# Performance work log

Hardware: AMD Instinct MI355X
Metric: run time of the kernel (lower is better)

## Reference

```python
import jax, jax.numpy as jnp
import numpy as np
from jax import lax

B, D, H, STEPS = 16384, 256, 256, 25


def setup_inputs() -> dict:
    key = jax.random.key(0)
    k1, k2, k3, k4 = jax.random.split(key, 4)
    s1 = 1.0 / np.sqrt(D)
    s2 = 1.0 / np.sqrt(H)
    return {
        "z0": jax.random.normal(k1, (B, D), dtype=jnp.float32),
        "t_range": jnp.linspace(0.0, 1.0, STEPS, dtype=jnp.float32),
        "W1": jax.random.normal(k2, (D, H), dtype=jnp.float32) * s1,
        "b1": jnp.zeros((H,), dtype=jnp.float32),
        "wt": jax.random.normal(k3, (H,), dtype=jnp.float32) * 0.1,
        "W2": jax.random.normal(k4, (H, D), dtype=jnp.float32) * s2,
        "b2": jnp.zeros((D,), dtype=jnp.float32),
    }


def reference(z0, t_range, W1, b1, wt, W2, b2):
    # Euler solver: zt <- zt + dt * f(zt, t) for every t in t_range
    # (matches euler_solver: note it steps at ALL 25 grid points, incl. t_end)
    dt = t_range[1] - t_range[0]

    def dynamics(z, t):
        h = jnp.tanh(z @ W1 + b1 + t * wt)  # [B, H]
        return h @ W2 + b2                   # [B, D]

    def step(z, t):
        return z + dt * dynamics(z, t), None

    zT, _ = lax.scan(step, z0, t_range)
    return zT
```

## Files before the change

### kernel.cpp

```cpp
#include <hip/hip_runtime.h>

typedef short bf16x8 __attribute__((ext_vector_type(8)));
typedef float f32x4  __attribute__((ext_vector_type(4)));

#define NSTEP 25
#define SROW  264
#define LDSB  (32 * SROW)

__device__ __forceinline__ unsigned short f2bf(float x) {
    union { float f; unsigned int u; } v; v.f = x;
    unsigned int r = v.u + 0x7FFFu + ((v.u >> 16) & 1u);
    return (unsigned short)(r >> 16);
}

#if __has_builtin(__builtin_amdgcn_cvt_pk_bf16_f32)
typedef __bf16 bfv2 __attribute__((ext_vector_type(2)));
__device__ __forceinline__ unsigned int pk2bf(float a, float b) {
    union { bfv2 v; unsigned int u; } c;
    c.v = __builtin_amdgcn_cvt_pk_bf16_f32(a, b);
    return c.u;
}
#else
__device__ __forceinline__ unsigned int pk2bf(float a, float b) {
    return (unsigned int)f2bf(a) | ((unsigned int)f2bf(b) << 16);
}
#endif

__device__ __forceinline__ float tanh_fast(float x) {
    float e = __expf(2.0f * x);
    return 1.0f - 2.0f * __builtin_amdgcn_rcpf(e + 1.0f);
}

__global__ void prep_all(const float* __restrict__ W1,
                         const float* __restrict__ W2,
                         const float* __restrict__ b2,
                         const float* __restrict__ t_range,
                         unsigned short* __restrict__ Wr,
                         unsigned short* __restrict__ W21r,
                         float* __restrict__ c1)
{
    __shared__ float row[256];
    int b = blockIdx.x;
    if (b < 512) {
        const float* src = (b < 256) ? W1 : W2;
        unsigned short* dst = Wr + ((b < 256) ? 0 : 65536);
        int k = b & 255;
        int n = threadIdx.x;
        int p  = (k & ~31) | ((k & 15) << 1) | ((k >> 4) & 1);
        int kc = p >> 5, q = (p >> 3) & 3, j = p & 7;
        dst[kc * 8192 + n * 32 + q * 8 + j] = f2bf(src[k * 256 + n]);
    } else {
        int i = b - 512, j = threadIdx.x;
        row[j] = (i < 256) ? W2[i * 256 + j] : b2[j];
        __syncthreads();
        float acc = 0.f;
        for (int d = 0; d < 256; ++d)
            acc = fmaf(row[d], W1[d * 256 + j], acc);
        if (i < 256) {
            float dt = t_range[1] - t_range[0];
            int p  = (i & ~31) | ((i & 15) << 1) | ((i >> 4) & 1);
            int kc = p >> 5, q = (p >> 3) & 3, jj = p & 7;
            W21r[kc * 8192 + j * 32 + q * 8 + jj] = f2bf(dt * acc);
        } else {
            c1[j] = acc;
        }
    }
}

__global__ __launch_bounds__(512, 4) void ode_main(
    const float* __restrict__ z0,
    const float* __restrict__ t_range,
    const float* __restrict__ b1,
    const float* __restrict__ wt,
    const float* __restrict__ b2,
    const unsigned short* __restrict__ W1r,
    const unsigned short* __restrict__ W2r,
    const unsigned short* __restrict__ W21r,
    const float* __restrict__ c1,
    float* __restrict__ out)
{
    __shared__ __align__(16) unsigned short As[2 * LDSB];

    const int tid  = threadIdx.x;
    const int wave = tid >> 6;
    const int lane = tid & 63;
    const int q    = lane >> 4;
    const int l15  = lane & 15;
    const int row0 = blockIdx.x * 32;
    const int n0   = wave * 32;

    const float dt = t_range[1] - t_range[0];

    float bt[2], dbt[2];
#pragma unroll
    for (int tt = 0; tt < 2; ++tt) {
        int n = n0 + tt * 16 + l15;
        bt[tt]  = b1[n];
        dbt[tt] = dt * (wt[n] + c1[n]);
    }

#pragma unroll
    for (int band = 0; band < 2; ++band)
#pragma unroll
        for (int r = 0; r < 4; ++r) {
            int m = band * 16 + q * 4 + r;
            const float* zr = &z0[(row0 + m) * 256 + n0];
            *(unsigned int*)&As[m * SROW + n0 + l15 * 2] =
                pk2bf(zr[l15], zr[16 + l15]);
        }
    __syncthreads();

    f32x4 y[2][2];
#pragma unroll
    for (int band = 0; band < 2; ++band)
#pragma unroll
        for (int tt = 0; tt < 2; ++tt) y[band][tt] = f32x4{0.f, 0.f, 0.f, 0.f};
#pragma unroll
    for (int kc = 0; kc < 8; ++kc) {
        bf16x8 a[2];
#pragma unroll
        for (int band = 0; band < 2; ++band)
            a[band] = *(const bf16x8*)&As[(band * 16 + l15) * SROW + kc * 32 + q * 8];
#pragma unroll
        for (int tt = 0; tt < 2; ++tt) {
            bf16x8 bb = *(const bf16x8*)&W1r[kc * 8192 + (n0 + tt * 16 + l15) * 32 + q * 8];
#pragma unroll
            for (int band = 0; band < 2; ++band)
                y[band][tt] = __builtin_amdgcn_mfma_f32_16x16x32_bf16(
                    a[band], bb, y[band][tt], 0, 0, 0);
        }
    }

    bf16x8 w21f[8][2];
#pragma unroll
    for (int kc = 0; kc < 8; ++kc)
#pragma unroll
        for (int tt = 0; tt < 2; ++tt)
            w21f[kc][tt] = *(const bf16x8*)&W21r[kc * 8192 + (n0 + tt * 16 + l15) * 32 + q * 8];

    f32x4 S[2][2];
#pragma unroll
    for (int band = 0; band < 2; ++band)
#pragma unroll
        for (int tt = 0; tt < 2; ++tt) S[band][tt] = f32x4{0.f, 0.f, 0.f, 0.f};

    for (int s = 0; s < NSTEP - 1; ++s) {
        const int buf = ((s + 1) & 1) * LDSB;
#pragma unroll
        for (int band = 0; band < 2; ++band)
#pragma unroll
            for (int r = 0; r < 4; ++r) {
                int m = band * 16 + q * 4 + r;
                float h0 = tanh_fast(y[band][0][r] + bt[0]);
                float h1 = tanh_fast(y[band][1][r] + bt[1]);
                S[band][0][r] += h0; S[band][1][r] += h1;
                *(unsigned int*)&As[buf + m * SROW + n0 + l15 * 2] = pk2bf(h0, h1);
            }
        __syncthreads();

#pragma unroll
        for (int kc = 0; kc < 8; ++kc) {
            bf16x8 a[2];
#pragma unroll
            for (int band = 0; band < 2; ++band)
                a[band] = *(const bf16x8*)&As[buf + (band * 16 + l15) * SROW + kc * 32 + q * 8];
#pragma unroll
            for (int band = 0; band < 2; ++band)
#pragma unroll
                for (int tt = 0; tt < 2; ++tt)
                    y[band][tt] = __builtin_amdgcn_mfma_f32_16x16x32_bf16(
                        a[band], w21f[kc][tt], y[band][tt], 0, 0, 0);
        }

#pragma unroll
        for (int tt = 0; tt < 2; ++tt) bt[tt] += dbt[tt];
    }

#pragma unroll
    for (int band = 0; band < 2; ++band)
#pragma unroll
        for (int r = 0; r < 4; ++r)
#pragma unroll
            for (int tt = 0; tt < 2; ++tt)
                S[band][tt][r] += tanh_fast(y[band][tt][r] + bt[tt]);

    {
        const int buf = LDSB;
#pragma unroll
        for (int band = 0; band < 2; ++band)
#pragma unroll
            for (int r = 0; r < 4; ++r) {
                int m = band * 16 + q * 4 + r;
                *(unsigned int*)&As[buf + m * SROW + n0 + l15 * 2] =
                    pk2bf(S[band][0][r], S[band][1][r]);
            }
        __syncthreads();

        f32x4 acc[2][2];
#pragma unroll
        for (int band = 0; band < 2; ++band)
#pragma unroll
            for (int tt = 0; tt < 2; ++tt) acc[band][tt] = f32x4{0.f, 0.f, 0.f, 0.f};
#pragma unroll
        for (int kc = 0; kc < 8; ++kc) {
            bf16x8 a[2];
#pragma unroll
            for (int band = 0; band < 2; ++band)
                a[band] = *(const bf16x8*)&As[buf + (band * 16 + l15) * SROW + kc * 32 + q * 8];
#pragma unroll
            for (int tt = 0; tt < 2; ++tt) {
                bf16x8 bb = *(const bf16x8*)&W2r[kc * 8192 + (n0 + tt * 16 + l15) * 32 + q * 8];
#pragma unroll
                for (int band = 0; band < 2; ++band)
                    acc[band][tt] = __builtin_amdgcn_mfma_f32_16x16x32_bf16(
                        a[band], bb, acc[band][tt], 0, 0, 0);
            }
        }

        const float cb2 = (float)NSTEP * dt;
#pragma unroll
        for (int band = 0; band < 2; ++band)
#pragma unroll
            for (int tt = 0; tt < 2; ++tt) {
                float b2v = b2[n0 + tt * 16 + l15];
#pragma unroll
                for (int r = 0; r < 4; ++r) {
                    int idx = (row0 + band * 16 + q * 4 + r) * 256 + n0 + tt * 16 + l15;
                    out[idx] = z0[idx] + dt * acc[band][tt][r] + cb2 * b2v;
                }
            }
    }
}

extern "C" void kernel_launch(void* const* d_in, const int* in_sizes, int n_in,
                              void* d_out, int out_size, void* d_ws, size_t ws_size,
                              hipStream_t stream) {
    const float* z0      = (const float*)d_in[0];
    const float* t_range = (const float*)d_in[1];
    const float* W1      = (const float*)d_in[2];
    const float* b1      = (const float*)d_in[3];
    const float* wt      = (const float*)d_in[4];
    const float* W2      = (const float*)d_in[5];
    const float* b2      = (const float*)d_in[6];

    unsigned short* Wr = (unsigned short*)d_ws;
    unsigned short* W1r  = Wr;
    unsigned short* W2r  = Wr + 65536;
    unsigned short* W21r = Wr + 131072;
    float*          c1   = (float*)(Wr + 196608);

    prep_all<<<769, 256, 0, stream>>>(W1, W2, b2, t_range, Wr, W21r, c1);
    ode_main<<<512, 512, 0, stream>>>(z0, t_range, b1, wt, b2,
                                      W1r, W2r, W21r, c1, (float*)d_out);
}
```

Measured before the change: 152.9 us.

## Replace block barriers with per-wave LDS flags and rotated k-chunk order

Each __syncthreads in the ODE loop is replaced by per-wave monotonic flags in LDS. Each wave publishes its slice of the tanh activations and starts the MFMA reduction on its own k-chunk first, then spin-waits with s_sleep only for the other chunks it needs. The goal is to cut the full-block barrier stall each Euler step, so fast waves can overlap with slow ones. The W21 fragment loads move before the first GEMM, and the prep reduction gets four independent accumulators to shorten its dependency chain. The spin-wait polling and fences may cost more than the barriers they replace.

```diff
diff --git a/kernel.cpp b/kernel.cpp
--- a/kernel.cpp
+++ b/kernel.cpp
@@ -29,6 +29,12 @@
 __device__ __forceinline__ float tanh_fast(float x) {
     float e = __expf(2.0f * x);
     return 1.0f - 2.0f * __builtin_amdgcn_rcpf(e + 1.0f);
+}
+
+__device__ __forceinline__ void wait_flag(const unsigned int* f, unsigned int v) {
+    while (__hip_atomic_load(f, __ATOMIC_RELAXED, __HIP_MEMORY_SCOPE_WORKGROUP) < v)
+        __builtin_amdgcn_s_sleep(1);
+    __threadfence_block();
 }
 
 __global__ void prep_all(const float* __restrict__ W1,
@@ -53,9 +59,14 @@
         int i = b - 512, j = threadIdx.x;
         row[j] = (i < 256) ? W2[i * 256 + j] : b2[j];
         __syncthreads();
-        float acc = 0.f;
-        for (int d = 0; d < 256; ++d)
-            acc = fmaf(row[d], W1[d * 256 + j], acc);
+        float a0 = 0.f, a1 = 0.f, a2 = 0.f, a3 = 0.f;
+        for (int d = 0; d < 256; d += 4) {
+            a0 = fmaf(row[d    ], W1[(d    ) * 256 + j], a0);
+            a1 = fmaf(row[d + 1], W1[(d + 1) * 256 + j], a1);
+            a2 = fmaf(row[d + 2], W1[(d + 2) * 256 + j], a2);
+            a3 = fmaf(row[d + 3], W1[(d + 3) * 256 + j], a3);
+        }
+        float acc = (a0 + a1) + (a2 + a3);
         if (i < 256) {
             float dt = t_range[1] - t_range[0];
             int p  = (i & ~31) | ((i & 15) << 1) | ((i >> 4) & 1);
@@ -80,6 +91,7 @@
     float* __restrict__ out)
 {
     __shared__ __align__(16) unsigned short As[2 * LDSB];
+    __shared__ unsigned int flags[8];
 
     const int tid  = threadIdx.x;
     const int wave = tid >> 6;
@@ -89,8 +101,9 @@
     const int row0 = blockIdx.x * 32;
     const int n0   = wave * 32;
 
+    if (tid < 8) flags[tid] = 0;
+
     const float dt = t_range[1] - t_range[0];
-
     float bt[2], dbt[2];
 #pragma unroll
     for (int tt = 0; tt < 2; ++tt) {
@@ -98,6 +111,8 @@
         bt[tt]  = b1[n];
         dbt[tt] = dt * (wt[n] + c1[n]);
     }
+
+    __syncthreads();
 
 #pragma unroll
     for (int band = 0; band < 2; ++band)
@@ -108,7 +123,18 @@
             *(unsigned int*)&As[m * SROW + n0 + l15 * 2] =
                 pk2bf(zr[l15], zr[16 + l15]);
         }
-    __syncthreads();
+    __threadfence_block();
+    if (lane == 0)
+        __hip_atomic_store(&flags[wave], 1u, __ATOMIC_RELAXED, __HIP_MEMORY_SCOPE_WORKGROUP);
+
+    bf16x8 w21f[8][2];
+#pragma unroll
+    for (int i = 0; i < 8; ++i) {
+        int kc = (wave + i) & 7;
+#pragma unroll
+        for (int tt = 0; tt < 2; ++tt)
+            w21f[i][tt] = *(const bf16x8*)&W21r[kc * 8192 + (n0 + tt * 16 + l15) * 32 + q * 8];
+    }
 
     f32x4 y[2][2];
 #pragma unroll
@@ -116,27 +142,18 @@
 #pragma unroll
         for (int tt = 0; tt < 2; ++tt) y[band][tt] = f32x4{0.f, 0.f, 0.f, 0.f};
 #pragma unroll
-    for (int kc = 0; kc < 8; ++kc) {
-        bf16x8 a[2];
-#pragma unroll
-        for (int band = 0; band < 2; ++band)
-            a[band] = *(const bf16x8*)&As[(band * 16 + l15) * SROW + kc * 32 + q * 8];
+    for (int i = 0; i < 8; ++i) {
+        int kc = (wave + i) & 7;
+        if (i > 0) wait_flag(&flags[kc], 1u);
+        bf16x8 a0 = *(const bf16x8*)&As[l15 * SROW + kc * 32 + q * 8];
+        bf16x8 a1 = *(const bf16x8*)&As[(16 + l15) * SROW + kc * 32 + q * 8];
 #pragma unroll
         for (int tt = 0; tt < 2; ++tt) {
             bf16x8 bb = *(const bf16x8*)&W1r[kc * 8192 + (n0 + tt * 16 + l15) * 32 + q * 8];
-#pragma unroll
-            for (int band = 0; band < 2; ++band)
-                y[band][tt] = __builtin_amdgcn_mfma_f32_16x16x32_bf16(
-                    a[band], bb, y[band][tt], 0, 0, 0);
-        }
-    }
-
-    bf16x8 w21f[8][2];
-#pragma unroll
-    for (int kc = 0; kc < 8; ++kc)
-#pragma unroll
-        for (int tt = 0; tt < 2; ++tt)
-            w21f[kc][tt] = *(const bf16x8*)&W21r[kc * 8192 + (n0 + tt * 16 + l15) * 32 + q * 8];
+            y[0][tt] = __builtin_amdgcn_mfma_f32_16x16x32_bf16(a0, bb, y[0][tt], 0, 0, 0);
+            y[1][tt] = __builtin_amdgcn_mfma_f32_16x16x32_bf16(a1, bb, y[1][tt], 0, 0, 0);
+        }
+    }
 
     f32x4 S[2][2];
 #pragma unroll
@@ -146,6 +163,8 @@
 
     for (int s = 0; s < NSTEP - 1; ++s) {
         const int buf = ((s + 1) & 1) * LDSB;
+        const unsigned int fv = (unsigned int)(s + 2);
+
 #pragma unroll
         for (int band = 0; band < 2; ++band)
 #pragma unroll
@@ -156,20 +175,20 @@
                 S[band][0][r] += h0; S[band][1][r] += h1;
                 *(unsigned int*)&As[buf + m * SROW + n0 + l15 * 2] = pk2bf(h0, h1);
             }
-        __syncthreads();
-
-#pragma unroll
-        for (int kc = 0; kc < 8; ++kc) {
-            bf16x8 a[2];
-#pragma unroll
-            for (int band = 0; band < 2; ++band)
-                a[band] = *(const bf16x8*)&As[buf + (band * 16 + l15) * SROW + kc * 32 + q * 8];
-#pragma unroll
-            for (int band = 0; band < 2; ++band)
-#pragma unroll
-                for (int tt = 0; tt < 2; ++tt)
-                    y[band][tt] = __builtin_amdgcn_mfma_f32_16x16x32_bf16(
-                        a[band], w21f[kc][tt], y[band][tt], 0, 0, 0);
+        __threadfence_block();
+        if (lane == 0)
+            __hip_atomic_store(&flags[wave], fv, __ATOMIC_RELAXED, __HIP_MEMORY_SCOPE_WORKGROUP);
+
+#pragma unroll
+        for (int i = 0; i < 8; ++i) {
+            int kc = (wave + i) & 7;
+            if (i > 0) wait_flag(&flags[kc], fv);
+            bf16x8 a0 = *(const bf16x8*)&As[buf + l15 * SROW + kc * 32 + q * 8];
+            bf16x8 a1 = *(const bf16x8*)&As[buf + (16 + l15) * SROW + kc * 32 + q * 8];
+            y[0][0] = __builtin_amdgcn_mfma_f32_16x16x32_bf16(a0, w21f[i][0], y[0][0], 0, 0, 0);
+            y[0][1] = __builtin_amdgcn_mfma_f32_16x16x32_bf16(a0, w21f[i][1], y[0][1], 0, 0, 0);
+            y[1][0] = __builtin_amdgcn_mfma_f32_16x16x32_bf16(a1, w21f[i][0], y[1][0], 0, 0, 0);
+            y[1][1] = __builtin_amdgcn_mfma_f32_16x16x32_bf16(a1, w21f[i][1], y[1][1], 0, 0, 0);
         }
 
 #pragma unroll
@@ -186,6 +205,7 @@
 
     {
         const int buf = LDSB;
+        const unsigned int fv = 26u;
 #pragma unroll
         for (int band = 0; band < 2; ++band)
 #pragma unroll
@@ -194,7 +214,9 @@
                 *(unsigned int*)&As[buf + m * SROW + n0 + l15 * 2] =
                     pk2bf(S[band][0][r], S[band][1][r]);
             }
-        __syncthreads();
+        __threadfence_block();
+        if (lane == 0)
+            __hip_atomic_store(&flags[wave], fv, __ATOMIC_RELAXED, __HIP_MEMORY_SCOPE_WORKGROUP);
 
         f32x4 acc[2][2];
 #pragma unroll
@@ -202,18 +224,16 @@
 #pragma unroll
             for (int tt = 0; tt < 2; ++tt) acc[band][tt] = f32x4{0.f, 0.f, 0.f, 0.f};
 #pragma unroll
-        for (int kc = 0; kc < 8; ++kc) {
-            bf16x8 a[2];
-#pragma unroll
-            for (int band = 0; band < 2; ++band)
-                a[band] = *(const bf16x8*)&As[buf + (band * 16 + l15) * SROW + kc * 32 + q * 8];
+        for (int i = 0; i < 8; ++i) {
+            int kc = (wave + i) & 7;
+            if (i > 0) wait_flag(&flags[kc], fv);
+            bf16x8 a0 = *(const bf16x8*)&As[buf + l15 * SROW + kc * 32 + q * 8];
+            bf16x8 a1 = *(const bf16x8*)&As[buf + (16 + l15) * SROW + kc * 32 + q * 8];
 #pragma unroll
             for (int tt = 0; tt < 2; ++tt) {
                 bf16x8 bb = *(const bf16x8*)&W2r[kc * 8192 + (n0 + tt * 16 + l15) * 32 + q * 8];
-#pragma unroll
-                for (int band = 0; band < 2; ++band)
-                    acc[band][tt] = __builtin_amdgcn_mfma_f32_16x16x32_bf16(
-                        a[band], bb, acc[band][tt], 0, 0, 0);
+                acc[0][tt] = __builtin_amdgcn_mfma_f32_16x16x32_bf16(a0, bb, acc[0][tt], 0, 0, 0);
+                acc[1][tt] = __builtin_amdgcn_mfma_f32_16x16x32_bf16(a1, bb, acc[1][tt], 0, 0, 0);
             }
         }
 
```

Result: slower. 193.8 us (+26.8%).
